# Performance work log

Measured on AMD Instinct MI355X. Metric: run time of the kernel, lower is better.

The kernel has to match this reference:

```python
import jax, jax.numpy as jnp
import numpy as np

NUM_HEADS = 16
NEG_INF = -1e30  # finite large negative; avoids NaN on fully-masked padded query rows


def setup_inputs() -> dict:
    key = jax.random.key(0)
    k0, k1, k2, k3 = jax.random.split(key, 4)
    B, S, E = 4, 2048, 1024
    x_padded = jax.random.normal(k0, (B, S, E), dtype=jnp.float32)
    # variable lengths in [S//2, S] so no batch row is fully empty
    seq_lengths = jax.random.randint(k1, (B,), S // 2, S + 1).astype(jnp.int32)
    Wqkv = jax.random.normal(k2, (3 * E, E), dtype=jnp.float32) * 0.02  # torch Linear weight [out,in]
    Wout = jax.random.normal(k3, (E, E), dtype=jnp.float32) * 0.02
    return {"x_padded": x_padded, "Wqkv": Wqkv, "Wout": Wout,
            "seq_lengths": seq_lengths, "window_left": 512, "window_right": 0}


def _build_mask(seq_lengths, S, window_left, window_right):
    # key-side padding mask: [B, S]
    pad = jnp.arange(S)[None, :] < seq_lengths[:, None]
    mask = pad[:, None, None, :]  # [B,1,1,S]
    if window_left >= 0 or window_right >= 0:
        i = jnp.arange(S)[:, None]
        j = jnp.arange(S)[None, :]
        win = jnp.ones((S, S), dtype=bool)
        if window_left >= 0:
            win = win & (j >= i - window_left)
        if window_right >= 0:
            win = win & (j <= i + window_right)
        mask = mask & win[None, None, :, :]
    elif (window_left, window_right) == (-1, 0):
        causal = jnp.tril(jnp.ones((S, S), dtype=bool))
        mask = mask & causal[None, None, :, :]
    return mask  # [B,1,S,S] (broadcasts over heads)


def reference(x_padded, Wqkv, Wout, seq_lengths, window_left, window_right):
    B, S, E = x_padded.shape
    H = NUM_HEADS
    D = E // H
    scale = 1.0 / jnp.sqrt(jnp.float32(D))
    qkv = x_padded @ Wqkv.T  # [B,S,3E]
    q, k, v = jnp.split(qkv, 3, axis=-1)
    q = q.reshape(B, S, H, D).transpose(0, 2, 1, 3)  # [B,H,S,D]
    k = k.reshape(B, S, H, D).transpose(0, 2, 1, 3)
    v = v.reshape(B, S, H, D).transpose(0, 2, 1, 3)
    mask = _build_mask(seq_lengths, S, window_left, window_right)
    scores = jnp.einsum("bhid,bhjd->bhij", q, k) * scale
    scores = jnp.where(mask, scores, NEG_INF)
    attn = jax.nn.softmax(scores, axis=-1)
    out = jnp.einsum("bhij,bhjd->bhid", attn, v)  # [B,H,S,D]
    out = out.transpose(0, 2, 1, 3).reshape(B, S, E)
    return out @ Wout.T
```

## Files before the change

kernel.cpp:

```cpp
#include <hip/hip_runtime.h>

typedef __bf16 bf16;
typedef __attribute__((ext_vector_type(2))) __bf16 bf16x2;
typedef __attribute__((ext_vector_type(4))) __bf16 bf16x4;
typedef __attribute__((ext_vector_type(8))) __bf16 bf16x8;
typedef __attribute__((ext_vector_type(4))) float f32x4;
typedef __attribute__((ext_vector_type(16))) float f32x16;

#define B_ 4
#define S_ 2048
#define H_ 16
#define D_ 64
#define E_ 1024

__device__ __forceinline__ int imin(int a, int b) { return a < b ? a : b; }
__device__ __forceinline__ int imax(int a, int b) { return a > b ? a : b; }

__device__ __forceinline__ void gload_lds16(const void* g, void* l) {
  __builtin_amdgcn_global_load_lds(
      (const __attribute__((address_space(1))) void*)g,
      (__attribute__((address_space(3))) void*)l, 16, 0, 0);
}

__global__ __launch_bounds__(256) void f32_to_bf16_kernel(
    const float* __restrict__ in, bf16* __restrict__ out, int n) {
  int i = (blockIdx.x * 256 + threadIdx.x) * 8;
  const int stride = gridDim.x * 256 * 8;
  for (; i < n; i += stride) {
    float4 v0 = *(const float4*)(in + i);
    float4 v1 = *(const float4*)(in + i + 4);
    bf16x8 o;
    o[0] = (bf16)v0.x; o[1] = (bf16)v0.y; o[2] = (bf16)v0.z; o[3] = (bf16)v0.w;
    o[4] = (bf16)v1.x; o[5] = (bf16)v1.y; o[6] = (bf16)v1.z; o[7] = (bf16)v1.w;
    *(bf16x8*)(out + i) = o;
  }
}

__global__ __launch_bounds__(256) void gemm_nt(
    const bf16* __restrict__ A, const bf16* __restrict__ Bm,
    int M, int N, int K, int mode,
    bf16* __restrict__ qd, bf16* __restrict__ kd, bf16* __restrict__ vtd,
    float* __restrict__ outf) {
  __shared__ __align__(16) bf16 As[128 * 64];
  __shared__ __align__(16) bf16 Bs[128 * 64];
  const int tid = threadIdx.x;
  const int wave = tid >> 6, lane = tid & 63;
  const int l15 = lane & 15, l4 = lane >> 4;
  const int tn = blockIdx.x, tm = blockIdx.y;
  const int wm = (wave >> 1) * 64, wn = (wave & 1) * 64;

  f32x4 acc[4][4];
#pragma unroll
  for (int i = 0; i < 4; ++i)
#pragma unroll
    for (int j = 0; j < 4; ++j)
#pragma unroll
      for (int r = 0; r < 4; ++r) acc[i][j][r] = 0.f;

  const bf16* Abase = A + (size_t)tm * 128 * K;
  const bf16* Bbase = Bm + (size_t)tn * 128 * K;

  for (int k0 = 0; k0 < K; k0 += 64) {
#pragma unroll
    for (int it = 0; it < 4; ++it) {
      const int gidx = it * 256 + tid;
      const int row = gidx >> 3, c = gidx & 7;
      const int csw = c ^ (row & 7);
      gload_lds16(Abase + (size_t)row * K + k0 + csw * 8,
                  As + (size_t)(it * 256 + wave * 64) * 8);
      gload_lds16(Bbase + (size_t)row * K + k0 + csw * 8,
                  Bs + (size_t)(it * 256 + wave * 64) * 8);
    }
    __syncthreads();
#pragma unroll
    for (int kc = 0; kc < 2; ++kc) {
      bf16x8 af[4], bfr[4];
#pragma unroll
      for (int i = 0; i < 4; ++i) {
        const int ra = wm + i * 16 + l15;
        af[i] = *(const bf16x8*)(As + ra * 64 + (((kc * 4 + l4) ^ (ra & 7)) * 8));
        const int rb = wn + i * 16 + l15;
        bfr[i] = *(const bf16x8*)(Bs + rb * 64 + (((kc * 4 + l4) ^ (rb & 7)) * 8));
      }
#pragma unroll
      for (int i = 0; i < 4; ++i)
#pragma unroll
        for (int j = 0; j < 4; ++j)
          acc[i][j] = __builtin_amdgcn_mfma_f32_16x16x32_bf16(af[i], bfr[j],
                                                              acc[i][j], 0, 0, 0);
    }
    __syncthreads();
  }

  if (mode == 0) {
#pragma unroll
    for (int i = 0; i < 4; ++i) {
      const int m0 = tm * 128 + wm + i * 16 + l4 * 4;
      const int b = m0 >> 11, s = m0 & (S_ - 1);
#pragma unroll
      for (int j = 0; j < 4; ++j) {
        const int n = tn * 128 + wn + j * 16 + l15;
        const int which = n >> 10;
        const int hn = n & 1023;
        const int h = hn >> 6, d = hn & 63;
        const f32x4 a = acc[i][j];
        if (which == 0) {
#pragma unroll
          for (int r = 0; r < 4; ++r)
            qd[((size_t)(b * H_ + h) * S_ + (s + r)) * D_ + d] =
                (bf16)(a[r] * 0.125f);
        } else if (which == 1) {
#pragma unroll
          for (int r = 0; r < 4; ++r)
            kd[((size_t)(b * H_ + h) * S_ + (s + r)) * D_ + d] = (bf16)a[r];
        } else {
          bf16x4 pv;
#pragma unroll
          for (int r = 0; r < 4; ++r) pv[r] = (bf16)a[r];
          *(bf16x4*)(vtd + ((size_t)(b * H_ + h) * D_ + d) * S_ + s) = pv;
        }
      }
    }
  } else {
#pragma unroll
    for (int i = 0; i < 4; ++i) {
      const int m0 = tm * 128 + wm + i * 16 + l4 * 4;
#pragma unroll
      for (int j = 0; j < 4; ++j) {
        const int n = tn * 128 + wn + j * 16 + l15;
#pragma unroll
        for (int r = 0; r < 4; ++r) outf[(size_t)(m0 + r) * N + n] = acc[i][j][r];
      }
    }
  }
}

__global__ __launch_bounds__(256) void meanv_kernel(const bf16* __restrict__ vt,
                                                    float* __restrict__ meanv) {
  __shared__ float part[256];
  const int bh = blockIdx.x;
  const int tid = threadIdx.x;
  const int d = tid & 63, seg = tid >> 6;
  const bf16* row = vt + ((size_t)bh * D_ + d) * S_ + seg * 512;
  float s = 0.f;
  for (int i = 0; i < 512; i += 8) {
    bf16x8 v = *(const bf16x8*)(row + i);
#pragma unroll
    for (int j = 0; j < 8; ++j) s += (float)v[j];
  }
  part[tid] = s;
  __syncthreads();
  if (tid < 64) {
    float t = part[tid] + part[64 + tid] + part[128 + tid] + part[192 + tid];
    meanv[(size_t)bh * D_ + tid] = t * (1.0f / (float)S_);
  }
}

__device__ __forceinline__ int pk2(float a, float b) {
  union { bf16x2 h; int i; } u;
  u.h[0] = (bf16)a; u.h[1] = (bf16)b;
  return u.i;
}

__global__ __launch_bounds__(128) void attn_kernel(
    const bf16* __restrict__ q, const bf16* __restrict__ k,
    const bf16* __restrict__ vt, const float* __restrict__ meanv,
    const int* __restrict__ seq_lengths, const int* __restrict__ wlp,
    const int* __restrict__ wrp, bf16* __restrict__ attn_out) {
  __shared__ float Lm[64], Ll[64];
  __shared__ float Lo[32][64];
  const int tid = threadIdx.x, wave = tid >> 6, lane = tid & 63;
  const int l31 = lane & 31, l5 = lane >> 5;
  const int bid0 = blockIdx.x;
  const int bid = (bid0 & 7) * 512 + (bid0 >> 3);
  const int bh = bid >> 6;
  const int g = bid & 63;
  const int b = bh >> 4, h = bh & 15;
  const int q0w = g * 32;
  const int seq_len = seq_lengths[b];
  const int wl = wlp[0], wr = wrp[0];

  const bf16* qbase = q + (size_t)bh * S_ * D_;
  const bf16* kbase = k + (size_t)bh * S_ * D_;
  const bf16* vtb = vt + (size_t)bh * D_ * S_;

  bf16x8 qa[4];
#pragma unroll
  for (int dg = 0; dg < 4; ++dg)
    qa[dg] = *(const bf16x8*)(qbase + (size_t)(q0w + l31) * D_ + dg * 16 + l5 * 8);

  const int hi_ = (wr >= 0) ? imin(q0w + 31 + wr, S_ - 1) : (S_ - 1);
  const int kv_end = imin(hi_ + 1, seq_len);
  const int lo_ = (wl >= 0) ? imax(0, q0w - wl) : 0;
  const int kv_begin = lo_ & ~31;
  const int span = kv_end - kv_begin;
  const int nt = (span > 0) ? ((span + 31) >> 5) : 0;

  f32x16 o0, o1;
#pragma unroll
  for (int r = 0; r < 16; ++r) { o0[r] = 0.f; o1[r] = 0.f; }
  float mrun = -1e30f, lrun = 0.f;

  int kt0 = kv_begin + wave * 32;
  if (wave >= nt) kt0 = kv_begin;
  bf16x8 kreg[4];
#pragma unroll
  for (int dg = 0; dg < 4; ++dg)
    kreg[dg] = *(const bf16x8*)(kbase + (size_t)(kt0 + l31) * D_ + dg * 16 + l5 * 8);

  for (int t = wave; t < nt; t += 2) {
    const int kt = kv_begin + t * 32;
    f32x16 sf;
#pragma unroll
    for (int r = 0; r < 16; ++r) sf[r] = 0.f;
#pragma unroll
    for (int dg = 0; dg < 4; ++dg)
      sf = __builtin_amdgcn_mfma_f32_32x32x16_bf16(kreg[dg], qa[dg], sf, 0, 0, 0);

    bf16x8 vreg[4];
#pragma unroll
    for (int kg = 0; kg < 2; ++kg) {
      vreg[kg * 2 + 0] = *(const bf16x8*)(vtb + (size_t)(l31) * S_ + kt + kg * 16 + l5 * 8);
      vreg[kg * 2 + 1] = *(const bf16x8*)(vtb + (size_t)(32 + l31) * S_ + kt + kg * 16 + l5 * 8);
    }
    int ktn = kv_begin + (t + 2) * 32;
    if (t + 2 >= nt) ktn = kv_begin;
#pragma unroll
    for (int dg = 0; dg < 4; ++dg)
      kreg[dg] = *(const bf16x8*)(kbase + (size_t)(ktn + l31) * D_ + dg * 16 + l5 * 8);

    bool allv = (kt + 31 < seq_len);
    if (wr >= 0) allv = allv && (kt + 31 <= q0w + wr);
    if (wl >= 0) allv = allv && (kt >= q0w + 31 - wl);

    float p[16];
    float tmax = -1e30f;
    if (allv) {
#pragma unroll
      for (int r = 0; r < 16; ++r) { p[r] = sf[r]; tmax = fmaxf(tmax, p[r]); }
    } else {
      const int qrow = q0w + l31;
#pragma unroll
      for (int r = 0; r < 16; ++r) {
        const int key = kt + (r & 3) + 8 * (r >> 2) + 4 * l5;
        bool valid = (key < seq_len);
        if (wr >= 0) valid = valid && (key <= qrow + wr);
        if (wl >= 0) valid = valid && (key >= qrow - wl);
        p[r] = valid ? sf[r] : -1e30f;
        tmax = fmaxf(tmax, p[r]);
      }
    }
    tmax = fmaxf(tmax, __shfl_xor(tmax, 32, 64));

    if (!__all(tmax <= mrun + 8.0f)) {
      const float mnew = fmaxf(mrun, tmax);
      const float corr = __expf(mrun - mnew);
      mrun = mnew;
      lrun *= corr;
#pragma unroll
      for (int r = 0; r < 16; ++r) { o0[r] *= corr; o1[r] *= corr; }
    }

    float lsum = 0.f;
#pragma unroll
    for (int r = 0; r < 16; ++r) {
      const float pe = (p[r] <= -1e29f) ? 0.f : __expf(p[r] - mrun);
      p[r] = pe;
      lsum += pe;
    }
    lsum += __shfl_xor(lsum, 32, 64);
    lrun += lsum;

    bf16x8 pb[2];
#pragma unroll
    for (int kg = 0; kg < 2; ++kg) {
      const int w0 = pk2(p[kg * 8 + 0], p[kg * 8 + 1]);
      const int w1 = pk2(p[kg * 8 + 2], p[kg * 8 + 3]);
      const int w2 = pk2(p[kg * 8 + 4], p[kg * 8 + 5]);
      const int w3 = pk2(p[kg * 8 + 6], p[kg * 8 + 7]);
      auto r02 = __builtin_amdgcn_permlane32_swap(w0, w2, false, false);
      auto r13 = __builtin_amdgcn_permlane32_swap(w1, w3, false, false);
      union { int i[4]; bf16x8 v; } u;
      u.i[0] = r02[0]; u.i[1] = r13[0]; u.i[2] = r02[1]; u.i[3] = r13[1];
      pb[kg] = u.v;
    }

#pragma unroll
    for (int kg = 0; kg < 2; ++kg) {
      o0 = __builtin_amdgcn_mfma_f32_32x32x16_bf16(vreg[kg * 2 + 0], pb[kg], o0, 0, 0, 0);
      o1 = __builtin_amdgcn_mfma_f32_32x32x16_bf16(vreg[kg * 2 + 1], pb[kg], o1, 0, 0, 0);
    }
  }

  if (wave == 1) {
    Lm[lane] = mrun;
    Ll[lane] = lrun;
#pragma unroll
    for (int r = 0; r < 16; ++r) {
      Lo[r][lane] = o0[r];
      Lo[16 + r][lane] = o1[r];
    }
  }
  __syncthreads();
  if (wave == 1) return;

  const float m2 = Lm[lane], l2 = Ll[lane];
  const float ms = fmaxf(mrun, m2);
  const float w1 = __expf(mrun - ms), w2 = __expf(m2 - ms);
  const float ls = lrun * w1 + l2 * w2;
#pragma unroll
  for (int r = 0; r < 16; ++r) {
    o0[r] = o0[r] * w1 + Lo[r][lane] * w2;
    o1[r] = o1[r] * w1 + Lo[16 + r][lane] * w2;
  }

  const int qrow = q0w + l31;
  bf16* outp = attn_out + ((size_t)(b * S_ + qrow)) * E_ + h * 64;
  if (ls > 0.f) {
    const float inv = 1.0f / ls;
#pragma unroll
    for (int dg2 = 0; dg2 < 2; ++dg2) {
      const f32x16& o = dg2 ? o1 : o0;
#pragma unroll
      for (int rg = 0; rg < 4; ++rg) {
        const int d0 = dg2 * 32 + 8 * rg + 4 * l5;
        bf16x4 ov;
#pragma unroll
        for (int j = 0; j < 4; ++j) ov[j] = (bf16)(o[rg * 4 + j] * inv);
        *(bf16x4*)(outp + d0) = ov;
      }
    }
  } else {
    const float* mv = meanv + (size_t)bh * D_;
#pragma unroll
    for (int dg2 = 0; dg2 < 2; ++dg2)
#pragma unroll
      for (int rg = 0; rg < 4; ++rg) {
        const int d0 = dg2 * 32 + 8 * rg + 4 * l5;
        bf16x4 ov;
#pragma unroll
        for (int j = 0; j < 4; ++j) ov[j] = (bf16)mv[d0 + j];
        *(bf16x4*)(outp + d0) = ov;
      }
  }
}

extern "C" void kernel_launch(void* const* d_in, const int* in_sizes, int n_in,
                              void* d_out, int out_size, void* d_ws, size_t ws_size,
                              hipStream_t stream) {
  const float* x = (const float*)d_in[0];
  const float* Wqkv = (const float*)d_in[1];
  const float* Wout = (const float*)d_in[2];
  const int* seq_lengths = (const int*)d_in[3];
  const int* wl = (const int*)d_in[4];
  const int* wr = (const int*)d_in[5];
  float* out = (float*)d_out;

  char* ws = (char*)d_ws;
  bf16* xb = (bf16*)ws;      ws += (size_t)8192 * 1024 * 2;
  bf16* wqkvb = (bf16*)ws;   ws += (size_t)3072 * 1024 * 2;
  bf16* woutb = (bf16*)ws;   ws += (size_t)1024 * 1024 * 2;
  bf16* qd = (bf16*)ws;      ws += (size_t)B_ * H_ * S_ * D_ * 2;
  bf16* kd = (bf16*)ws;      ws += (size_t)B_ * H_ * S_ * D_ * 2;
  bf16* vtd = (bf16*)ws;     ws += (size_t)B_ * H_ * S_ * D_ * 2;
  bf16* attn = (bf16*)ws;    ws += (size_t)8192 * 1024 * 2;
  float* meanv = (float*)ws; ws += (size_t)B_ * H_ * D_ * 4;

  f32_to_bf16_kernel<<<2048, 256, 0, stream>>>(x, xb, 8192 * 1024);
  f32_to_bf16_kernel<<<768, 256, 0, stream>>>(Wqkv, wqkvb, 3072 * 1024);
  f32_to_bf16_kernel<<<512, 256, 0, stream>>>(Wout, woutb, 1024 * 1024);

  gemm_nt<<<dim3(24, 64), 256, 0, stream>>>(xb, wqkvb, 8192, 3072, 1024, 0,
                                            qd, kd, vtd, nullptr);
  meanv_kernel<<<64, 256, 0, stream>>>(vtd, meanv);
  attn_kernel<<<4096, 128, 0, stream>>>(qd, kd, vtd, meanv, seq_lengths, wl, wr,
                                        attn);
  gemm_nt<<<dim3(8, 64), 256, 0, stream>>>(attn, woutb, 8192, 1024, 1024, 1,
                                           nullptr, nullptr, nullptr, out);
}
```

Baseline: 192.5 us.

## Replace GEMM with triple-buffered 256x128 pipelined kernel and XCD-aware tile swizzle

Both projection GEMMs now use a new kernel with 512 threads, a 256x128 block tile and a three-stage LDS ring. Global-to-LDS loads for tile t+2 are issued between the MFMA halves, with vmcnt waits and a single barrier per iteration, so loads overlap compute and the second syncthreads is gone. It also adds a new LDS XOR swizzle, s_setprio around the MFMA bursts, and a block-index remap that groups workgroups by fid&7, presumably for XCD and L2 locality. The cost is more LDS (about 144KB), one block per CU, and fewer workgroups. The tail iterations reload the last tile redundantly.

```diff
diff --git a/kernel.cpp b/kernel.cpp
--- a/kernel.cpp
+++ b/kernel.cpp
@@ -12,6 +12,10 @@
 #define H_ 16
 #define D_ 64
 #define E_ 1024
+
+#define BM 256
+#define BN 128
+#define BK 64
 
 __device__ __forceinline__ int imin(int a, int b) { return a < b ? a : b; }
 __device__ __forceinline__ int imax(int a, int b) { return a > b ? a : b; }
@@ -36,18 +40,28 @@
   }
 }
 
-__global__ __launch_bounds__(256) void gemm_nt(
+__global__ __launch_bounds__(512, 1) void gemm_pipe(
     const bf16* __restrict__ A, const bf16* __restrict__ Bm,
     int M, int N, int K, int mode,
     bf16* __restrict__ qd, bf16* __restrict__ kd, bf16* __restrict__ vtd,
     float* __restrict__ outf) {
-  __shared__ __align__(16) bf16 As[128 * 64];
-  __shared__ __align__(16) bf16 Bs[128 * 64];
+  __shared__ __align__(16) bf16 As[3][BM * BK];
+  __shared__ __align__(16) bf16 Bs[3][BN * BK];
   const int tid = threadIdx.x;
   const int wave = tid >> 6, lane = tid & 63;
   const int l15 = lane & 15, l4 = lane >> 4;
-  const int tn = blockIdx.x, tm = blockIdx.y;
-  const int wm = (wave >> 1) * 64, wn = (wave & 1) * 64;
+  const int wm = (wave >> 1) * 64;
+  const int wn = (wave & 1) * 64;
+
+  const int nwg = gridDim.x * gridDim.y;
+  const int fid = blockIdx.y * gridDim.x + blockIdx.x;
+  const int chunk = nwg >> 3;
+  const int swz = (fid & 7) * chunk + (fid >> 3);
+  const int tn = swz % gridDim.x;
+  const int tm = swz / gridDim.x;
+
+  const bf16* Abase = A + (size_t)tm * BM * K;
+  const bf16* Bbase = Bm + (size_t)tn * BN * K;
 
   f32x4 acc[4][4];
 #pragma unroll
@@ -57,66 +71,107 @@
 #pragma unroll
       for (int r = 0; r < 4; ++r) acc[i][j][r] = 0.f;
 
-  const bf16* Abase = A + (size_t)tm * 128 * K;
-  const bf16* Bbase = Bm + (size_t)tn * 128 * K;
-
-  for (int k0 = 0; k0 < K; k0 += 64) {
-#pragma unroll
-    for (int it = 0; it < 4; ++it) {
-      const int gidx = it * 256 + tid;
-      const int row = gidx >> 3, c = gidx & 7;
-      const int csw = c ^ (row & 7);
-      gload_lds16(Abase + (size_t)row * K + k0 + csw * 8,
-                  As + (size_t)(it * 256 + wave * 64) * 8);
-      gload_lds16(Bbase + (size_t)row * K + k0 + csw * 8,
-                  Bs + (size_t)(it * 256 + wave * 64) * 8);
-    }
-    __syncthreads();
-#pragma unroll
-    for (int kc = 0; kc < 2; ++kc) {
-      bf16x8 af[4], bfr[4];
-#pragma unroll
-      for (int i = 0; i < 4; ++i) {
-        const int ra = wm + i * 16 + l15;
-        af[i] = *(const bf16x8*)(As + ra * 64 + (((kc * 4 + l4) ^ (ra & 7)) * 8));
-        const int rb = wn + i * 16 + l15;
-        bfr[i] = *(const bf16x8*)(Bs + rb * 64 + (((kc * 4 + l4) ^ (rb & 7)) * 8));
-      }
-#pragma unroll
-      for (int i = 0; i < 4; ++i)
-#pragma unroll
-        for (int j = 0; j < 4; ++j)
-          acc[i][j] = __builtin_amdgcn_mfma_f32_16x16x32_bf16(af[i], bfr[j],
-                                                              acc[i][j], 0, 0, 0);
-    }
-    __syncthreads();
-  }
+  const int NT = K >> 6;
+
+#define STAGE_A(sbuf, k0)                                                      \
+  {                                                                            \
+    _Pragma("unroll") for (int ld = 0; ld < 4; ++ld) {                         \
+      const int idx = ld * 512 + tid;                                          \
+      const int row = idx >> 3, g = idx & 7;                                   \
+      const int gs = g ^ (((row >> 2) & 1) << 1);                              \
+      gload_lds16(Abase + (size_t)row * K + (k0) + gs * 8,                     \
+                  As[sbuf] + (ld * 512 + wave * 64) * 8);                      \
+    }                                                                          \
+  }
+#define STAGE_B(sbuf, k0)                                                      \
+  {                                                                            \
+    _Pragma("unroll") for (int ld = 0; ld < 2; ++ld) {                         \
+      const int idx = ld * 512 + tid;                                          \
+      const int row = idx >> 3, g = idx & 7;                                   \
+      const int gs = g ^ (((row >> 2) & 1) << 1);                              \
+      gload_lds16(Bbase + (size_t)row * K + (k0) + gs * 8,                     \
+                  Bs[sbuf] + (ld * 512 + wave * 64) * 8);                      \
+    }                                                                          \
+  }
+
+  STAGE_A(0, 0); STAGE_B(0, 0);
+  STAGE_A(1, BK); STAGE_B(1, BK);
+  asm volatile("s_waitcnt vmcnt(6)" ::: "memory");
+  __builtin_amdgcn_s_barrier();
+
+  int p = 0;
+  for (int t = 0; t < NT; ++t) {
+    const bf16* Ap = As[p];
+    const bf16* Bp = Bs[p];
+    const int sb = (p + 2 >= 3) ? p - 1 : p + 2;
+    const int sk0 = ((t + 2 < NT) ? t + 2 : NT - 1) * BK;
+
+    bf16x8 a[4], bfr[4];
+#pragma unroll
+    for (int i = 0; i < 4; ++i) {
+      const int ra = wm + i * 16 + l15;
+      a[i] = *(const bf16x8*)(Ap + ra * 64 + ((l4 * 8) ^ (((ra >> 2) & 1) << 4)));
+      const int rb = wn + i * 16 + l15;
+      bfr[i] = *(const bf16x8*)(Bp + rb * 64 + ((l4 * 8) ^ (((rb >> 2) & 1) << 4)));
+    }
+    STAGE_A(sb, sk0);
+    __builtin_amdgcn_s_setprio(1);
+#pragma unroll
+    for (int i = 0; i < 4; ++i)
+#pragma unroll
+      for (int j = 0; j < 4; ++j)
+        acc[i][j] = __builtin_amdgcn_mfma_f32_16x16x32_bf16(a[i], bfr[j],
+                                                            acc[i][j], 0, 0, 0);
+    __builtin_amdgcn_s_setprio(0);
+#pragma unroll
+    for (int i = 0; i < 4; ++i) {
+      const int ra = wm + i * 16 + l15;
+      a[i] = *(const bf16x8*)(Ap + ra * 64 + ((32 + l4 * 8) ^ (((ra >> 2) & 1) << 4)));
+      const int rb = wn + i * 16 + l15;
+      bfr[i] = *(const bf16x8*)(Bp + rb * 64 + ((32 + l4 * 8) ^ (((rb >> 2) & 1) << 4)));
+    }
+    STAGE_B(sb, sk0);
+    __builtin_amdgcn_s_setprio(1);
+#pragma unroll
+    for (int i = 0; i < 4; ++i)
+#pragma unroll
+      for (int j = 0; j < 4; ++j)
+        acc[i][j] = __builtin_amdgcn_mfma_f32_16x16x32_bf16(a[i], bfr[j],
+                                                            acc[i][j], 0, 0, 0);
+    __builtin_amdgcn_s_setprio(0);
+
+    asm volatile("s_waitcnt vmcnt(6)" ::: "memory");
+    __builtin_amdgcn_s_barrier();
+    p = (p + 1 >= 3) ? 0 : p + 1;
+  }
+#undef STAGE_A
+#undef STAGE_B
 
   if (mode == 0) {
 #pragma unroll
     for (int i = 0; i < 4; ++i) {
-      const int m0 = tm * 128 + wm + i * 16 + l4 * 4;
+      const int m0 = tm * BM + wm + i * 16 + l4 * 4;
       const int b = m0 >> 11, s = m0 & (S_ - 1);
 #pragma unroll
       for (int j = 0; j < 4; ++j) {
-        const int n = tn * 128 + wn + j * 16 + l15;
+        const int n = tn * BN + wn + j * 16 + l15;
         const int which = n >> 10;
         const int hn = n & 1023;
         const int h = hn >> 6, d = hn & 63;
-        const f32x4 a = acc[i][j];
+        const f32x4 av = acc[i][j];
         if (which == 0) {
 #pragma unroll
           for (int r = 0; r < 4; ++r)
             qd[((size_t)(b * H_ + h) * S_ + (s + r)) * D_ + d] =
-                (bf16)(a[r] * 0.125f);
+                (bf16)(av[r] * 0.125f);
         } else if (which == 1) {
 #pragma unroll
           for (int r = 0; r < 4; ++r)
-            kd[((size_t)(b * H_ + h) * S_ + (s + r)) * D_ + d] = (bf16)a[r];
+            kd[((size_t)(b * H_ + h) * S_ + (s + r)) * D_ + d] = (bf16)av[r];
         } else {
           bf16x4 pv;
 #pragma unroll
-          for (int r = 0; r < 4; ++r) pv[r] = (bf16)a[r];
+          for (int r = 0; r < 4; ++r) pv[r] = (bf16)av[r];
           *(bf16x4*)(vtd + ((size_t)(b * H_ + h) * D_ + d) * S_ + s) = pv;
         }
       }
@@ -124,10 +179,10 @@
   } else {
 #pragma unroll
     for (int i = 0; i < 4; ++i) {
-      const int m0 = tm * 128 + wm + i * 16 + l4 * 4;
+      const int m0 = tm * BM + wm + i * 16 + l4 * 4;
 #pragma unroll
       for (int j = 0; j < 4; ++j) {
-        const int n = tn * 128 + wn + j * 16 + l15;
+        const int n = tn * BN + wn + j * 16 + l15;
 #pragma unroll
         for (int r = 0; r < 4; ++r) outf[(size_t)(m0 + r) * N + n] = acc[i][j][r];
       }
@@ -370,11 +425,11 @@
   f32_to_bf16_kernel<<<768, 256, 0, stream>>>(Wqkv, wqkvb, 3072 * 1024);
   f32_to_bf16_kernel<<<512, 256, 0, stream>>>(Wout, woutb, 1024 * 1024);
 
-  gemm_nt<<<dim3(24, 64), 256, 0, stream>>>(xb, wqkvb, 8192, 3072, 1024, 0,
-                                            qd, kd, vtd, nullptr);
+  gemm_pipe<<<dim3(24, 32), 512, 0, stream>>>(xb, wqkvb, 8192, 3072, 1024, 0,
+                                              qd, kd, vtd, nullptr);
   meanv_kernel<<<64, 256, 0, stream>>>(vtd, meanv);
   attn_kernel<<<4096, 128, 0, stream>>>(qd, kd, vtd, meanv, seq_lengths, wl, wr,
                                         attn);
-  gemm_nt<<<dim3(8, 64), 256, 0, stream>>>(attn, woutb, 8192, 1024, 1024, 1,
-                                           nullptr, nullptr, nullptr, out);
-}
+  gemm_pipe<<<dim3(8, 32), 512, 0, stream>>>(attn, woutb, 8192, 1024, 1024, 1,
+                                             nullptr, nullptr, nullptr, out);
+}
```

Measured after the change: 187.7 us. 2.5% less time.
